# Optimization experiments

Hardware: AMD Instinct MI355X
Metric: run time of the kernel (lower is better)

## Reference

```python
import jax, jax.numpy as jnp
import numpy as np

B, N, K = 4, 8192, 32
HID, INP = 64, 64
IN_CH = HID + INP  # 128; SetConv fc1 sees IN_CH + 3 (relative pos)


def setup_inputs() -> dict:
    key = jax.random.key(0)
    ks = jax.random.split(key, 10)
    return {
        "h": jax.random.normal(ks[0], (B, N, HID), jnp.float32),
        "x": jax.random.normal(ks[1], (B, N, INP), jnp.float32),
        "c": jax.random.normal(ks[2], (B, N, 3), jnp.float32),
        "W1": jax.random.normal(ks[3], (3, IN_CH + 3, HID), jnp.float32) * 0.05,
        "b1": jnp.zeros((3, HID), jnp.float32),
        "W2": jax.random.normal(ks[4], (3, HID, HID), jnp.float32) * 0.05,
        "b2": jnp.zeros((3, HID), jnp.float32),
        "W3": jax.random.normal(ks[5], (3, HID, HID), jnp.float32) * 0.05,
        "b3": jnp.zeros((3, HID), jnp.float32),
        "neigh_idx": jax.random.randint(ks[6], (B, N, K), 0, N, jnp.int32),
        "edge_feats": jax.random.normal(ks[7], (B, N, K, 3), jnp.float32),
    }


def reference(h, x, c, W1, b1, W2, b2, W3, b3, neigh_idx, edge_feats):
    # c (point coordinates) is unused by the GRU body, matching the torch source.
    slope = 0.1

    def setconv(i, feat):
        # gather K neighbor features per point: [B, N, K, C]
        g = jax.vmap(lambda fb, ib: fb[ib])(feat, neigh_idx)
        e = jnp.concatenate([g, edge_feats], axis=-1)  # [B, N, K, C+3]
        y = jax.nn.leaky_relu(jnp.einsum('bnkc,cd->bnkd', e, W1[i]) + b1[i], slope)
        y = y.max(axis=2)  # pool over neighbors -> [B, N, HID]
        y = jax.nn.leaky_relu(y @ W2[i] + b2[i], slope)
        return y @ W3[i] + b3[i]

    hx = jnp.concatenate([h, x], axis=2)
    z = jax.nn.sigmoid(setconv(0, hx))
    r = jax.nn.sigmoid(setconv(1, hx))
    q = jnp.tanh(setconv(2, jnp.concatenate([r * h, x], axis=2)))
    return (1.0 - z) * h + z * q
```

## Files before the change

kernel.cpp:

```cpp
#include <hip/hip_runtime.h>
#include <math.h>

typedef unsigned short u16;
typedef unsigned int u32;
typedef __attribute__((ext_vector_type(8))) short s8v;
typedef __attribute__((ext_vector_type(4))) float f4v;

#define KNBR 32
#define MFMA16(a, b, c) __builtin_amdgcn_mfma_f32_16x16x32_bf16((a), (b), (c), 0, 0, 0)

__device__ __forceinline__ float bf2f(u16 u) { return __uint_as_float((u32)u << 16); }
__device__ __forceinline__ float bflo(u32 u) { return __uint_as_float(u << 16); }
__device__ __forceinline__ float bfhi(u32 u) { return __uint_as_float(u & 0xffff0000u); }
__device__ __forceinline__ u16 f2bf(float f) {
    u32 u = __float_as_uint(f);
    return (u16)((u + 0x7fffu + ((u >> 16) & 1u)) >> 16);
}
__device__ __forceinline__ u32 pk2(float a, float b) {
    return (u32)f2bf(a) | ((u32)f2bf(b) << 16);
}
__device__ __forceinline__ float leaky(float v) { return v >= 0.f ? v : 0.1f * v; }
__device__ __forceinline__ float sigm(float v) { return 1.f / (1.f + expf(-v)); }

__device__ __forceinline__ int swz_plb(int b, int full) {
    if (!full) return b << 6;
    int xcd = b & 7;
    int within = ((b >> 3) << 1) | (xcd & 1);
    return ((xcd >> 1) << 13) + (within << 6);
}


__global__ __launch_bounds__(512) void k_gemm_p01(
    const float* __restrict__ h, const float* __restrict__ x,
    const float* __restrict__ W1f, const float* __restrict__ b1f,
    u32* __restrict__ P01, int p0, int full)
{
    __shared__ u32 a_lds[64 * 68];
    __shared__ u32 wb[2 * 64 * 68];
    int t = threadIdx.x;
    int plb = swz_plb(blockIdx.x, full);
    int pgb = p0 + plb;
    for (int i = 0; i < 8; ++i) {
        int id = t + i * 512;
        int p = id >> 6, cw = id & 63;
        const float* src = (cw < 32) ? (h + (size_t)(pgb + p) * 64 + cw * 2)
                                     : (x + (size_t)(pgb + p) * 64 + (cw - 32) * 2);
        float2 v = *(const float2*)src;
        a_lds[p * 68 + cw] = pk2(v.x, v.y);
    }
    for (int i = 0; i < 16; ++i) {
        int id = t + i * 512;
        int g = id >> 12, kp = (id >> 6) & 63, n = id & 63;
        float w0 = W1f[g * 8384 + kp * 128 + n];
        float w1 = W1f[g * 8384 + kp * 128 + 64 + n];
        wb[(g * 64 + n) * 68 + kp] = pk2(w0, w1);
    }
    __syncthreads();
    int lane = t & 63;
    int w = __builtin_amdgcn_readfirstlane(t >> 6);
    int m = w & 3, npair = w >> 2;
    int quad = lane >> 4, l15 = lane & 15;
    f4v acc[2][2];
    #pragma unroll
    for (int g = 0; g < 2; ++g)
        #pragma unroll
        for (int nt = 0; nt < 2; ++nt) {
            float b = b1f[g * 64 + (npair * 2 + nt) * 16 + l15];
            acc[g][nt] = (f4v){b, b, b, b};
        }
    #pragma unroll
    for (int kb = 0; kb < 4; ++kb) {
        s8v af = *(const s8v*)&a_lds[(m * 16 + l15) * 68 + kb * 16 + quad * 4];
        #pragma unroll
        for (int g = 0; g < 2; ++g)
            #pragma unroll
            for (int nt = 0; nt < 2; ++nt) {
                s8v bf = *(const s8v*)&wb[(g * 64 + (npair * 2 + nt) * 16 + l15) * 68
                                          + kb * 16 + quad * 4];
                acc[g][nt] = MFMA16(af, bf, acc[g][nt]);
            }
    }
    #pragma unroll
    for (int nt = 0; nt < 2; ++nt)
        #pragma unroll
        for (int r = 0; r < 4; ++r) {
            int pt = m * 16 + quad * 4 + r;
            int ch = (npair * 2 + nt) * 16 + l15;
            P01[(size_t)(plb + pt) * 64 + ch] = pk2(acc[0][nt][r], acc[1][nt][r]);
        }
}

__global__ __launch_bounds__(512) void k_fuse01(
    const u32* __restrict__ P01, const float* __restrict__ W1f,
    const int* __restrict__ nidx, const float* __restrict__ ef,
    const float* __restrict__ h, const float* __restrict__ x,
    const float* __restrict__ W2f, const float* __restrict__ b2f,
    const float* __restrict__ W3f, const float* __restrict__ b3f,
    const float* __restrict__ b1f,
    u16* __restrict__ Z, float* __restrict__ P2, int p0, int full)
{
    __shared__ u32 a_lds[64 * 68];
    __shared__ u32 wb[4608];
    int t = threadIdx.x;
    int plb = swz_plb(blockIdx.x, full);
    int lane = t & 63;
    int w = __builtin_amdgcn_readfirstlane(t >> 6);
    int quad = lane >> 4, l15 = lane & 15;
    u16* y16 = (u16*)a_lds;

    for (int i = 0; i < 8; ++i) {
        int id = t + i * 512;
        int g = id >> 11, kp = (id >> 6) & 31, n = id & 63;
        float w0 = W2f[g * 4096 + kp * 128 + n];
        float w1 = W2f[g * 4096 + kp * 128 + 64 + n];
        wb[(g * 64 + n) * 36 + kp] = pk2(w0, w1);
    }
    {
        float w00 = W1f[8192 + lane], w01 = W1f[8256 + lane], w02 = W1f[8320 + lane];
        float w10 = W1f[16576 + lane], w11 = W1f[16640 + lane], w12 = W1f[16704 + lane];
        for (int pp = 0; pp < 8; ++pp) {
            int lp = w * 8 + pp;
            int pg = p0 + plb + lp;
            int rbase = ((pg >> 13) << 13) - p0;
            const int* ni = nidx + (size_t)pg * KNBR;
            const float* ep = ef + (size_t)pg * KNBR * 3;
            float m0 = -1e30f, m1 = -1e30f;
            #pragma unroll 16
            for (int k = 0; k < KNBR; ++k) {
                int lr = rbase + ni[k];
                u32 gv = P01[(size_t)lr * 64 + lane];
                float e0 = ep[3 * k], e1 = ep[3 * k + 1], e2 = ep[3 * k + 2];
                m0 = fmaxf(m0, bflo(gv) + e0 * w00 + e1 * w01 + e2 * w02);
                m1 = fmaxf(m1, bfhi(gv) + e0 * w10 + e1 * w11 + e2 * w12);
            }
            y16[lp * 136 + lane]      = f2bf(leaky(m0));
            y16[lp * 136 + 64 + lane] = f2bf(leaky(m1));
        }
    }
    __syncthreads();
    int m = w & 3, g = w >> 2;
    f4v acc[4];
    #pragma unroll
    for (int nt = 0; nt < 4; ++nt) {
        float b = b2f[g * 64 + nt * 16 + l15];
        acc[nt] = (f4v){b, b, b, b};
    }
    #pragma unroll
    for (int kb = 0; kb < 2; ++kb) {
        s8v af = *(const s8v*)&a_lds[(m * 16 + l15) * 68 + g * 32 + kb * 16 + quad * 4];
        #pragma unroll
        for (int nt = 0; nt < 4; ++nt) {
            s8v bf = *(const s8v*)&wb[(g * 64 + nt * 16 + l15) * 36 + kb * 16 + quad * 4];
            acc[nt] = MFMA16(af, bf, acc[nt]);
        }
    }
    #pragma unroll
    for (int nt = 0; nt < 4; ++nt)
        #pragma unroll
        for (int r = 0; r < 4; ++r)
            y16[(m * 16 + quad * 4 + r) * 136 + g * 64 + nt * 16 + l15] =
                f2bf(leaky(acc[nt][r]));
    __syncthreads();
    for (int i = 0; i < 8; ++i) {
        int id = t + i * 512;
        int gg = id >> 11, kp = (id >> 6) & 31, n = id & 63;
        float w0 = W3f[gg * 4096 + kp * 128 + n];
        float w1 = W3f[gg * 4096 + kp * 128 + 64 + n];
        wb[(gg * 64 + n) * 36 + kp] = pk2(w0, w1);
    }
    __syncthreads();
    #pragma unroll
    for (int nt = 0; nt < 4; ++nt) {
        float b = b3f[g * 64 + nt * 16 + l15];
        acc[nt] = (f4v){b, b, b, b};
    }
    #pragma unroll
    for (int kb = 0; kb < 2; ++kb) {
        s8v af = *(const s8v*)&a_lds[(m * 16 + l15) * 68 + g * 32 + kb * 16 + quad * 4];
        #pragma unroll
        for (int nt = 0; nt < 4; ++nt) {
            s8v bf = *(const s8v*)&wb[(g * 64 + nt * 16 + l15) * 36 + kb * 16 + quad * 4];
            acc[nt] = MFMA16(af, bf, acc[nt]);
        }
    }
    __syncthreads();
    if (g == 0) {
        #pragma unroll
        for (int nt = 0; nt < 4; ++nt)
            #pragma unroll
            for (int r = 0; r < 4; ++r) {
                int pt = m * 16 + quad * 4 + r;
                int ch = nt * 16 + l15;
                Z[(size_t)(plb + pt) * 64 + ch] = f2bf(sigm(acc[nt][r]));
            }
    } else {
        #pragma unroll
        for (int nt = 0; nt < 4; ++nt)
            #pragma unroll
            for (int r = 0; r < 4; ++r) {
                int pt = m * 16 + quad * 4 + r;
                int ch = nt * 16 + l15;
                float hv = h[(size_t)(p0 + plb + pt) * 64 + ch];
                y16[pt * 136 + ch] = f2bf(sigm(acc[nt][r]) * hv);
            }
    }
    for (int i = 0; i < 4; ++i) {
        int id = t + i * 512;
        int p = id >> 5, cw = id & 31;
        float2 v = *(const float2*)(x + (size_t)(p0 + plb + p) * 64 + cw * 2);
        a_lds[p * 68 + 32 + cw] = pk2(v.x, v.y);
    }
    for (int i = 0; i < 8; ++i) {
        int id = t + i * 512;
        int kp = (id >> 6) & 63, n = id & 63;
        float w0 = W1f[2 * 8384 + kp * 128 + n];
        float w1 = W1f[2 * 8384 + kp * 128 + 64 + n];
        wb[n * 68 + kp] = pk2(w0, w1);
    }
    __syncthreads();
    int nh = w >> 2;
    f4v pacc[2];
    #pragma unroll
    for (int nt = 0; nt < 2; ++nt) {
        float b = b1f[128 + (nh * 2 + nt) * 16 + l15];
        pacc[nt] = (f4v){b, b, b, b};
    }
    #pragma unroll
    for (int kb = 0; kb < 4; ++kb) {
        s8v af = *(const s8v*)&a_lds[(m * 16 + l15) * 68 + kb * 16 + quad * 4];
        #pragma unroll
        for (int nt = 0; nt < 2; ++nt) {
            s8v bf = *(const s8v*)&wb[((nh * 2 + nt) * 16 + l15) * 68 + kb * 16 + quad * 4];
            pacc[nt] = MFMA16(af, bf, pacc[nt]);
        }
    }
    #pragma unroll
    for (int nt = 0; nt < 2; ++nt)
        #pragma unroll
        for (int r = 0; r < 4; ++r) {
            int pt = m * 16 + quad * 4 + r;
            int ch = (nh * 2 + nt) * 16 + l15;
            P2[(size_t)(plb + pt) * 64 + ch] = pacc[nt][r];
        }
}

__global__ __launch_bounds__(512) void k_fuse2(
    const float* __restrict__ P2, const float* __restrict__ W1f,
    const int* __restrict__ nidx, const float* __restrict__ ef,
    const float* __restrict__ W2f, const float* __restrict__ b2f,
    const float* __restrict__ W3f, const float* __restrict__ b3f,
    const float* __restrict__ h, const u16* __restrict__ Z,
    float* __restrict__ out, int p0, int full)
{
    __shared__ u32 a_lds[64 * 36];
    __shared__ u32 wb[64 * 36];
    int t = threadIdx.x;
    int plb = swz_plb(blockIdx.x, full);
    int lane = t & 63;
    int w = __builtin_amdgcn_readfirstlane(t >> 6);
    int quad = lane >> 4, l15 = lane & 15;
    u16* y16 = (u16*)a_lds;

    for (int i = 0; i < 4; ++i) {
        int id = t + i * 512;
        int kp = (id >> 6) & 31, n = id & 63;
        float w0 = W2f[2 * 4096 + kp * 128 + n];
        float w1 = W2f[2 * 4096 + kp * 128 + 64 + n];
        wb[n * 36 + kp] = pk2(w0, w1);
    }
    {
        const float* W = W1f + 2 * 8384;
        float w0 = W[8192 + lane], w1 = W[8256 + lane], w2 = W[8320 + lane];
        for (int pp = 0; pp < 8; ++pp) {
            int lp = w * 8 + pp;
            int pg = p0 + plb + lp;
            int rbase = ((pg >> 13) << 13) - p0;
            const int* ni = nidx + (size_t)pg * KNBR;
            const float* ep = ef + (size_t)pg * KNBR * 3;
            float m = -1e30f;
            #pragma unroll 16
            for (int k = 0; k < KNBR; ++k) {
                int lr = rbase + ni[k];
                float e0 = ep[3 * k], e1 = ep[3 * k + 1], e2 = ep[3 * k + 2];
                float v = P2[(size_t)lr * 64 + lane] + e0 * w0 + e1 * w1 + e2 * w2;
                m = fmaxf(m, v);
            }
            y16[lp * 72 + lane] = f2bf(leaky(m));
        }
    }
    __syncthreads();
    int m = w & 3, nh = w >> 2;
    f4v acc[2];
    #pragma unroll
    for (int nt = 0; nt < 2; ++nt) {
        float b = b2f[128 + (nh * 2 + nt) * 16 + l15];
        acc[nt] = (f4v){b, b, b, b};
    }
    #pragma unroll
    for (int kb = 0; kb < 2; ++kb) {
        s8v af = *(const s8v*)&a_lds[(m * 16 + l15) * 36 + kb * 16 + quad * 4];
        #pragma unroll
        for (int nt = 0; nt < 2; ++nt) {
            s8v bf = *(const s8v*)&wb[((nh * 2 + nt) * 16 + l15) * 36 + kb * 16 + quad * 4];
            acc[nt] = MFMA16(af, bf, acc[nt]);
        }
    }
    __syncthreads();
    #pragma unroll
    for (int nt = 0; nt < 2; ++nt)
        #pragma unroll
        for (int r = 0; r < 4; ++r)
            y16[(m * 16 + quad * 4 + r) * 72 + (nh * 2 + nt) * 16 + l15] =
                f2bf(leaky(acc[nt][r]));
    for (int i = 0; i < 4; ++i) {
        int id = t + i * 512;
        int kp = (id >> 6) & 31, n = id & 63;
        float w0 = W3f[2 * 4096 + kp * 128 + n];
        float w1 = W3f[2 * 4096 + kp * 128 + 64 + n];
        wb[n * 36 + kp] = pk2(w0, w1);
    }
    __syncthreads();
    #pragma unroll
    for (int nt = 0; nt < 2; ++nt) {
        float b = b3f[128 + (nh * 2 + nt) * 16 + l15];
        acc[nt] = (f4v){b, b, b, b};
    }
    #pragma unroll
    for (int kb = 0; kb < 2; ++kb) {
        s8v af = *(const s8v*)&a_lds[(m * 16 + l15) * 36 + kb * 16 + quad * 4];
        #pragma unroll
        for (int nt = 0; nt < 2; ++nt) {
            s8v bf = *(const s8v*)&wb[((nh * 2 + nt) * 16 + l15) * 36 + kb * 16 + quad * 4];
            acc[nt] = MFMA16(af, bf, acc[nt]);
        }
    }
    #pragma unroll
    for (int nt = 0; nt < 2; ++nt)
        #pragma unroll
        for (int r = 0; r < 4; ++r) {
            int pt = m * 16 + quad * 4 + r;
            int ch = (nh * 2 + nt) * 16 + l15;
            int pl = plb + pt;
            int pg = p0 + pl;
            float z = bf2f(Z[(size_t)pl * 64 + ch]);
            float hv = h[(size_t)pg * 64 + ch];
            out[(size_t)pg * 64 + ch] = (1.f - z) * hv + z * tanhf(acc[nt][r]);
        }
}

extern "C" void kernel_launch(void* const* d_in, const int* in_sizes, int n_in,
                              void* d_out, int out_size, void* d_ws, size_t ws_size,
                              hipStream_t stream)
{
    const float* h  = (const float*)d_in[0];
    const float* x  = (const float*)d_in[1];
    const float* W1 = (const float*)d_in[3];
    const float* b1 = (const float*)d_in[4];
    const float* W2 = (const float*)d_in[5];
    const float* b2 = (const float*)d_in[6];
    const float* W3 = (const float*)d_in[7];
    const float* b3 = (const float*)d_in[8];
    const int* nidx = (const int*)d_in[9];
    const float* ef = (const float*)d_in[10];
    float* out = (float*)d_out;

    char* wsb = (char*)d_ws;
    size_t PN = (ws_size >= 32768ull * 640ull) ? 32768 : 8192;
    int passes = (int)(32768 / PN);
    int full = (PN == 32768) ? 1 : 0;

    u32* P01  = (u32*)wsb;
    u16* Z    = (u16*)(wsb + PN * 256);
    float* P2 = (float*)(wsb + PN * 384);

    for (int s = 0; s < passes; ++s) {
        int p0 = (int)(s * PN);
        dim3 g((unsigned)(PN / 64));
        k_gemm_p01<<<g, 512, 0, stream>>>(h, x, W1, b1, P01, p0, full);
        k_fuse01  <<<g, 512, 0, stream>>>(P01, W1, nidx, ef, h, x,
                                          W2, b2, W3, b3, b1, Z, P2, p0, full);
        k_fuse2   <<<g, 512, 0, stream>>>(P2, W1, nidx, ef,
                                          W2, b2, W3, b3, h, Z, out, p0, full);
    }
}
```

Measured before the change: 182.8 us.

## Pre-pack bf16 weight tiles once and stage neighbor indices/edge feats in LDS

Adds a prep kernel that converts all W1/W2/W3 slices to padded, transposed bf16 tiles in workspace once per call. Each kernel then copies those tiles into LDS with plain coalesced loads instead of doing strided fp32 gathers and packing per block. The fuse kernels also bulk-load each block's neighbor indices and edge features into LDS up front, with edge features packed partly to bf16, so the gather loop reads them from LDS. This costs an extra launch, more LDS per block (possibly lower occupancy), and some precision loss on two edge-feature components.

Measured after the change: 195.6 us. +7.0%, slower.

```diff
diff --git a/kernel.cpp b/kernel.cpp
--- a/kernel.cpp
+++ b/kernel.cpp
@@ -29,14 +29,64 @@
     return ((xcd >> 1) << 13) + (within << 6);
 }
 
+#define T2O 8704
+#define T3O 13056
+#define T4O 17664
+#define T5O 22272
+#define T6O 24576
+#define TTOT 26880
+
+__global__ __launch_bounds__(512) void k_prep(
+    const float* __restrict__ W1f, const float* __restrict__ W2f,
+    const float* __restrict__ W3f, u32* __restrict__ TB)
+{
+    int id = blockIdx.x * 512 + threadIdx.x;
+    if (id >= TTOT) return;
+    u32 word = 0;
+    if (id < T2O) {
+        int g = id / 4352, r = id - g * 4352;
+        int n = r / 68, kp = r - n * 68;
+        if (kp < 64)
+            word = pk2(W1f[g * 8384 + kp * 128 + n], W1f[g * 8384 + kp * 128 + 64 + n]);
+    } else if (id < T3O) {
+        int r = id - T2O;
+        int n = r / 68, kp = r - n * 68;
+        if (kp < 64)
+            word = pk2(W1f[16768 + kp * 128 + n], W1f[16768 + kp * 128 + 64 + n]);
+    } else if (id < T4O) {
+        int r = id - T3O;
+        int g = r / 2304, r2 = r - g * 2304;
+        int n = r2 / 36, kp = r2 - n * 36;
+        if (kp < 32)
+            word = pk2(W2f[g * 4096 + kp * 128 + n], W2f[g * 4096 + kp * 128 + 64 + n]);
+    } else if (id < T5O) {
+        int r = id - T4O;
+        int g = r / 2304, r2 = r - g * 2304;
+        int n = r2 / 36, kp = r2 - n * 36;
+        if (kp < 32)
+            word = pk2(W3f[g * 4096 + kp * 128 + n], W3f[g * 4096 + kp * 128 + 64 + n]);
+    } else if (id < T6O) {
+        int r = id - T5O;
+        int n = r / 36, kp = r - n * 36;
+        if (kp < 32)
+            word = pk2(W2f[8192 + kp * 128 + n], W2f[8192 + kp * 128 + 64 + n]);
+    } else {
+        int r = id - T6O;
+        int n = r / 36, kp = r - n * 36;
+        if (kp < 32)
+            word = pk2(W3f[8192 + kp * 128 + n], W3f[8192 + kp * 128 + 64 + n]);
+    }
+    TB[id] = word;
+}
+
 
 __global__ __launch_bounds__(512) void k_gemm_p01(
     const float* __restrict__ h, const float* __restrict__ x,
-    const float* __restrict__ W1f, const float* __restrict__ b1f,
+    const u32* __restrict__ TB, const float* __restrict__ b1f,
     u32* __restrict__ P01, int p0, int full)
 {
     __shared__ u32 a_lds[64 * 68];
-    __shared__ u32 wb[2 * 64 * 68];
+    __shared__ u32 wb[8704];
     int t = threadIdx.x;
     int plb = swz_plb(blockIdx.x, full);
     int pgb = p0 + plb;
@@ -48,13 +98,7 @@
         float2 v = *(const float2*)src;
         a_lds[p * 68 + cw] = pk2(v.x, v.y);
     }
-    for (int i = 0; i < 16; ++i) {
-        int id = t + i * 512;
-        int g = id >> 12, kp = (id >> 6) & 63, n = id & 63;
-        float w0 = W1f[g * 8384 + kp * 128 + n];
-        float w1 = W1f[g * 8384 + kp * 128 + 64 + n];
-        wb[(g * 64 + n) * 68 + kp] = pk2(w0, w1);
-    }
+    for (int i = 0; i < 17; ++i) wb[t + i * 512] = TB[t + i * 512];
     __syncthreads();
     int lane = t & 63;
     int w = __builtin_amdgcn_readfirstlane(t >> 6);
@@ -92,44 +136,56 @@
 
 __global__ __launch_bounds__(512) void k_fuse01(
     const u32* __restrict__ P01, const float* __restrict__ W1f,
+    const u32* __restrict__ TB,
     const int* __restrict__ nidx, const float* __restrict__ ef,
     const float* __restrict__ h, const float* __restrict__ x,
-    const float* __restrict__ W2f, const float* __restrict__ b2f,
-    const float* __restrict__ W3f, const float* __restrict__ b3f,
-    const float* __restrict__ b1f,
+    const float* __restrict__ b1f, const float* __restrict__ b2f,
+    const float* __restrict__ b3f,
     u16* __restrict__ Z, float* __restrict__ P2, int p0, int full)
 {
     __shared__ u32 a_lds[64 * 68];
     __shared__ u32 wb[4608];
+    __shared__ u32 idx_l[2048];
+    __shared__ u32 ef_p[2048];
+    __shared__ float ef2f[2048];
     int t = threadIdx.x;
     int plb = swz_plb(blockIdx.x, full);
+    int pg0 = p0 + plb;
+    int rbase = ((pg0 >> 13) << 13) - p0;
     int lane = t & 63;
     int w = __builtin_amdgcn_readfirstlane(t >> 6);
     int quad = lane >> 4, l15 = lane & 15;
     u16* y16 = (u16*)a_lds;
 
-    for (int i = 0; i < 8; ++i) {
-        int id = t + i * 512;
-        int g = id >> 11, kp = (id >> 6) & 31, n = id & 63;
-        float w0 = W2f[g * 4096 + kp * 128 + n];
-        float w1 = W2f[g * 4096 + kp * 128 + 64 + n];
-        wb[(g * 64 + n) * 36 + kp] = pk2(w0, w1);
-    }
+    for (int i = 0; i < 9; ++i) wb[t + i * 512] = TB[T3O + t + i * 512];
+    for (int i = 0; i < 4; ++i) {
+        int cell = t + i * 512;
+        int pt = cell >> 5, k = cell & 31;
+        idx_l[cell] = (u32)(rbase + nidx[(size_t)(pg0 + pt) * KNBR + k]);
+    }
+    for (int i = 0; i < 4; ++i) {
+        int cell = t + i * 512;
+        int pt = cell >> 5, k = cell & 31;
+        const float* e = ef + ((size_t)(pg0 + pt) * KNBR + k) * 3;
+        ef_p[cell] = pk2(e[0], e[1]);
+        ef2f[cell] = e[2];
+    }
+    __syncthreads();
     {
         float w00 = W1f[8192 + lane], w01 = W1f[8256 + lane], w02 = W1f[8320 + lane];
         float w10 = W1f[16576 + lane], w11 = W1f[16640 + lane], w12 = W1f[16704 + lane];
         for (int pp = 0; pp < 8; ++pp) {
             int lp = w * 8 + pp;
-            int pg = p0 + plb + lp;
-            int rbase = ((pg >> 13) << 13) - p0;
-            const int* ni = nidx + (size_t)pg * KNBR;
-            const float* ep = ef + (size_t)pg * KNBR * 3;
+            const u32* ib = &idx_l[lp * 32];
+            const u32* eb = &ef_p[lp * 32];
+            const float* e2b = &ef2f[lp * 32];
             float m0 = -1e30f, m1 = -1e30f;
             #pragma unroll 16
             for (int k = 0; k < KNBR; ++k) {
-                int lr = rbase + ni[k];
-                u32 gv = P01[(size_t)lr * 64 + lane];
-                float e0 = ep[3 * k], e1 = ep[3 * k + 1], e2 = ep[3 * k + 2];
+                u32 row = ib[k];
+                u32 gv = P01[(size_t)row * 64 + lane];
+                u32 ew = eb[k];
+                float e0 = bflo(ew), e1 = bfhi(ew), e2 = e2b[k];
                 m0 = fmaxf(m0, bflo(gv) + e0 * w00 + e1 * w01 + e2 * w02);
                 m1 = fmaxf(m1, bfhi(gv) + e0 * w10 + e1 * w11 + e2 * w12);
             }
@@ -161,13 +217,7 @@
             y16[(m * 16 + quad * 4 + r) * 136 + g * 64 + nt * 16 + l15] =
                 f2bf(leaky(acc[nt][r]));
     __syncthreads();
-    for (int i = 0; i < 8; ++i) {
-        int id = t + i * 512;
-        int gg = id >> 11, kp = (id >> 6) & 31, n = id & 63;
-        float w0 = W3f[gg * 4096 + kp * 128 + n];
-        float w1 = W3f[gg * 4096 + kp * 128 + 64 + n];
-        wb[(gg * 64 + n) * 36 + kp] = pk2(w0, w1);
-    }
+    for (int i = 0; i < 9; ++i) wb[t + i * 512] = TB[T4O + t + i * 512];
     __syncthreads();
     #pragma unroll
     for (int nt = 0; nt < 4; ++nt) {
@@ -200,22 +250,19 @@
             for (int r = 0; r < 4; ++r) {
                 int pt = m * 16 + quad * 4 + r;
                 int ch = nt * 16 + l15;
-                float hv = h[(size_t)(p0 + plb + pt) * 64 + ch];
+                float hv = h[(size_t)(pg0 + pt) * 64 + ch];
                 y16[pt * 136 + ch] = f2bf(sigm(acc[nt][r]) * hv);
             }
     }
     for (int i = 0; i < 4; ++i) {
         int id = t + i * 512;
         int p = id >> 5, cw = id & 31;
-        float2 v = *(const float2*)(x + (size_t)(p0 + plb + p) * 64 + cw * 2);
+        float2 v = *(const float2*)(x + (size_t)(pg0 + p) * 64 + cw * 2);
         a_lds[p * 68 + 32 + cw] = pk2(v.x, v.y);
     }
-    for (int i = 0; i < 8; ++i) {
+    for (int i = 0; i < 9; ++i) {
         int id = t + i * 512;
-        int kp = (id >> 6) & 63, n = id & 63;
-        float w0 = W1f[2 * 8384 + kp * 128 + n];
-        float w1 = W1f[2 * 8384 + kp * 128 + 64 + n];
-        wb[n * 68 + kp] = pk2(w0, w1);
+        if (id < 4352) wb[id] = TB[T2O + id];
     }
     __syncthreads();
     int nh = w >> 2;
@@ -246,44 +293,59 @@
 
 __global__ __launch_bounds__(512) void k_fuse2(
     const float* __restrict__ P2, const float* __restrict__ W1f,
+    const u32* __restrict__ TB,
     const int* __restrict__ nidx, const float* __restrict__ ef,
-    const float* __restrict__ W2f, const float* __restrict__ b2f,
-    const float* __restrict__ W3f, const float* __restrict__ b3f,
+    const float* __restrict__ b2f, const float* __restrict__ b3f,
     const float* __restrict__ h, const u16* __restrict__ Z,
     float* __restrict__ out, int p0, int full)
 {
     __shared__ u32 a_lds[64 * 36];
-    __shared__ u32 wb[64 * 36];
+    __shared__ u32 wb[2304];
+    __shared__ u32 idx_l[2048];
+    __shared__ u32 ef_p[2048];
+    __shared__ float ef2f[2048];
     int t = threadIdx.x;
     int plb = swz_plb(blockIdx.x, full);
+    int pg0 = p0 + plb;
+    int rbase = ((pg0 >> 13) << 13) - p0;
     int lane = t & 63;
     int w = __builtin_amdgcn_readfirstlane(t >> 6);
     int quad = lane >> 4, l15 = lane & 15;
     u16* y16 = (u16*)a_lds;
 
+    for (int i = 0; i < 5; ++i) {
+        int id = t + i * 512;
+        if (id < 2304) wb[id] = TB[T5O + id];
+    }
     for (int i = 0; i < 4; ++i) {
-        int id = t + i * 512;
-        int kp = (id >> 6) & 31, n = id & 63;
-        float w0 = W2f[2 * 4096 + kp * 128 + n];
-        float w1 = W2f[2 * 4096 + kp * 128 + 64 + n];
-        wb[n * 36 + kp] = pk2(w0, w1);
-    }
+        int cell = t + i * 512;
+        int pt = cell >> 5, k = cell & 31;
+        idx_l[cell] = (u32)(rbase + nidx[(size_t)(pg0 + pt) * KNBR + k]);
+    }
+    for (int i = 0; i < 4; ++i) {
+        int cell = t + i * 512;
+        int pt = cell >> 5, k = cell & 31;
+        const float* e = ef + ((size_t)(pg0 + pt) * KNBR + k) * 3;
+        ef_p[cell] = pk2(e[0], e[1]);
+        ef2f[cell] = e[2];
+    }
+    __syncthreads();
     {
         const float* W = W1f + 2 * 8384;
         float w0 = W[8192 + lane], w1 = W[8256 + lane], w2 = W[8320 + lane];
         for (int pp = 0; pp < 8; ++pp) {
             int lp = w * 8 + pp;
-            int pg = p0 + plb + lp;
-            int rbase = ((pg >> 13) << 13) - p0;
-            const int* ni = nidx + (size_t)pg * KNBR;
-            const float* ep = ef + (size_t)pg * KNBR * 3;
+            const u32* ib = &idx_l[lp * 32];
+            const u32* eb = &ef_p[lp * 32];
+            const float* e2b = &ef2f[lp * 32];
             float m = -1e30f;
             #pragma unroll 16
             for (int k = 0; k < KNBR; ++k) {
-                int lr = rbase + ni[k];
-                float e0 = ep[3 * k], e1 = ep[3 * k + 1], e2 = ep[3 * k + 2];
-                float v = P2[(size_t)lr * 64 + lane] + e0 * w0 + e1 * w1 + e2 * w2;
-                m = fmaxf(m, v);
+                u32 row = ib[k];
+                float gv = P2[(size_t)row * 64 + lane];
+                u32 ew = eb[k];
+                float e0 = bflo(ew), e1 = bfhi(ew), e2 = e2b[k];
+                m = fmaxf(m, gv + e0 * w0 + e1 * w1 + e2 * w2);
             }
             y16[lp * 72 + lane] = f2bf(leaky(m));
         }
@@ -312,12 +374,9 @@
         for (int r = 0; r < 4; ++r)
             y16[(m * 16 + quad * 4 + r) * 72 + (nh * 2 + nt) * 16 + l15] =
                 f2bf(leaky(acc[nt][r]));
-    for (int i = 0; i < 4; ++i) {
+    for (int i = 0; i < 5; ++i) {
         int id = t + i * 512;
-        int kp = (id >> 6) & 31, n = id & 63;
-        float w0 = W3f[2 * 4096 + kp * 128 + n];
-        float w1 = W3f[2 * 4096 + kp * 128 + 64 + n];
-        wb[n * 36 + kp] = pk2(w0, w1);
+        if (id < 2304) wb[id] = TB[T6O + id];
     }
     __syncthreads();
     #pragma unroll
@@ -365,21 +424,24 @@
     float* out = (float*)d_out;
 
     char* wsb = (char*)d_ws;
-    size_t PN = (ws_size >= 32768ull * 640ull) ? 32768 : 8192;
+    size_t need_full = 32768ull * 640ull + (size_t)TTOT * 4ull;
+    size_t PN = (ws_size >= need_full) ? 32768 : 8192;
     int passes = (int)(32768 / PN);
     int full = (PN == 32768) ? 1 : 0;
 
     u32* P01  = (u32*)wsb;
     u16* Z    = (u16*)(wsb + PN * 256);
     float* P2 = (float*)(wsb + PN * 384);
-
+    u32* TB   = (u32*)(wsb + PN * 640);
+
+    k_prep<<<dim3((TTOT + 511) / 512), 512, 0, stream>>>(W1, W2, W3, TB);
     for (int s = 0; s < passes; ++s) {
         int p0 = (int)(s * PN);
         dim3 g((unsigned)(PN / 64));
-        k_gemm_p01<<<g, 512, 0, stream>>>(h, x, W1, b1, P01, p0, full);
-        k_fuse01  <<<g, 512, 0, stream>>>(P01, W1, nidx, ef, h, x,
-                                          W2, b2, W3, b3, b1, Z, P2, p0, full);
-        k_fuse2   <<<g, 512, 0, stream>>>(P2, W1, nidx, ef,
-                                          W2, b2, W3, b3, h, Z, out, p0, full);
-    }
-}
+        k_gemm_p01<<<g, 512, 0, stream>>>(h, x, TB, b1, P01, p0, full);
+        k_fuse01  <<<g, 512, 0, stream>>>(P01, W1, TB, nidx, ef, h, x,
+                                          b1, b2, b3, Z, P2, p0, full);
+        k_fuse2   <<<g, 512, 0, stream>>>(P2, W1, TB, nidx, ef,
+                                          b2, b3, h, Z, out, p0, full);
+    }
+}
```
